# Kernel optimization log

Hardware: AMD Instinct MI355X
Metric: run time of the kernel (lower is better)

The kernel has to match this reference:

```python
import jax, jax.numpy as jnp
import numpy as np

D_MODEL = 128
N_HEADS = 4
HEAD_DIM = D_MODEL // N_HEADS


def setup_inputs() -> dict:
    key = jax.random.key(0)
    ks = jax.random.split(key, 16)
    s = 0.05
    B, N, T = 1, 1024, 1024
    return {
        "node_states": jax.random.normal(ks[0], (B, N, D_MODEL), jnp.float32),
        "task_features": jax.random.normal(ks[1], (T, D_MODEL), jnp.float32),
        "in_proj_w": jax.random.normal(ks[2], (3 * D_MODEL, D_MODEL), jnp.float32) * s,
        "in_proj_b": jnp.zeros((3 * D_MODEL,), jnp.float32),
        "out_w": jax.random.normal(ks[3], (D_MODEL, D_MODEL), jnp.float32) * s,
        "out_b": jnp.zeros((D_MODEL,), jnp.float32),
        "W1": jax.random.normal(ks[4], (256, 256), jnp.float32) * s,
        "b1": jnp.zeros((256,), jnp.float32),
        "W2": jax.random.normal(ks[5], (128, 256), jnp.float32) * s,
        "b2": jnp.zeros((128,), jnp.float32),
        "W3": jax.random.normal(ks[6], (1, 128), jnp.float32) * s,
        "b3": jnp.zeros((1,), jnp.float32),
        "Wc1": jax.random.normal(ks[7], (256, D_MODEL), jnp.float32) * s,
        "bc1": jnp.zeros((256,), jnp.float32),
        "Wc2": jax.random.normal(ks[8], (32, 256), jnp.float32) * s,
        "bc2": jnp.zeros((32,), jnp.float32),
    }


def _mha(x, in_proj_w, in_proj_b, out_w, out_b):
    # x: [B, N, D]; torch nn.MultiheadAttention self-attention, batch_first.
    B, N, D = x.shape
    q = x @ in_proj_w[:D].T + in_proj_b[:D]
    k = x @ in_proj_w[D:2 * D].T + in_proj_b[D:2 * D]
    v = x @ in_proj_w[2 * D:].T + in_proj_b[2 * D:]
    def split(t):  # [B,N,D] -> [B,H,N,dh]
        return t.reshape(B, N, N_HEADS, HEAD_DIM).transpose(0, 2, 1, 3)
    qh, kh, vh = split(q), split(k), split(v)
    scores = jnp.einsum("bhqd,bhkd->bhqk", qh, kh) / jnp.sqrt(jnp.float32(HEAD_DIM))
    attn = jax.nn.softmax(scores, axis=-1)  # [B,H,N,N]
    ctx = jnp.einsum("bhqk,bhkd->bhqd", attn, vh)
    ctx = ctx.transpose(0, 2, 1, 3).reshape(B, N, D)
    out = ctx @ out_w.T + out_b
    attn_avg = attn.mean(axis=1)  # torch averages heads by default -> [B,N,N]
    return out, attn_avg


def reference(node_states, task_features, in_proj_w, in_proj_b, out_w, out_b,
              W1, b1, W2, b2, W3, b3, Wc1, bc1, Wc2, bc2):
    attended, attn_w = _mha(node_states, in_proj_w, in_proj_b, out_w, out_b)
    nodes = attended[0]  # original loop only uses batch 0: [N, D]
    # Linear on concat([task, node]) == split-weight sum; vectorize pairwise.
    t1 = task_features @ W1[:, :D_MODEL].T          # [T, 256]
    n1 = nodes @ W1[:, D_MODEL:].T                  # [N, 256]
    h1 = jax.nn.relu(t1[:, None, :] + n1[None, :, :] + b1)      # [T, N, 256]
    h2 = jax.nn.relu(jnp.einsum("tnc,kc->tnk", h1, W2) + b2)   # [T, N, 128]
    matching_scores = jax.nn.sigmoid(jnp.einsum("tnk,ok->tn", h2, W3) + b3[0])
    global_state = attended.mean(axis=1)            # [B, D]
    coordination_logits = jax.nn.relu(global_state @ Wc1.T + bc1) @ Wc2.T + bc2
    return matching_scores, coordination_logits, attn_w
```

## Files before the change

### kernel.cpp

```cpp
#include <hip/hip_runtime.h>
#include <hip/hip_fp16.h>
#include <stdint.h>


typedef __attribute__((ext_vector_type(4))) float floatx4;
typedef __attribute__((ext_vector_type(8))) _Float16 half8;

#define OFF_QKV  0x000000u
#define OFF_CTX  0x180000u
#define OFF_T1H  0x280000u
#define OFF_N1H  0x300000u
#define OFF_W2F  0x380000u
#define OFF_GS   0x398000u
#define OFF_SC   0x400000u
#define OFF_PG   0xC00000u

__device__ __forceinline__ unsigned pkadd(unsigned a, unsigned b) {
    unsigned r; asm("v_pk_add_f16 %0, %1, %2" : "=v"(r) : "v"(a), "v"(b)); return r;
}
__device__ __forceinline__ unsigned pkmax(unsigned a, unsigned b) {
    unsigned r; asm("v_pk_max_f16 %0, %1, %2" : "=v"(r) : "v"(a), "v"(b)); return r;
}
__device__ __forceinline__ unsigned pk2h(float a, float b) {
    return (unsigned)__half_as_ushort(__float2half(a)) |
           ((unsigned)__half_as_ushort(__float2half(b)) << 16);
}
__device__ __forceinline__ float h2f(unsigned short u) {
    return __half2float(__ushort_as_half(u));
}

template<bool BIAS, bool F16OUT>
__device__ __forceinline__ void gemm_dev(
    const float* __restrict__ A, int lda,
    const float* __restrict__ B, int ldb,
    const float* __restrict__ bias,
    void* __restrict__ Cv, int ldc, int K, float scale,
    int m0, int n0, float (*As)[64], float (*Bs)[64])
{
    const int tid = threadIdx.x;
    const int tx = tid & 15, ty = tid >> 4;
    const int lr = tid >> 2;
    const int lk = (tid & 3) * 4;
    float c[4][4] = {};

    for (int k0 = 0; k0 < K; k0 += 16) {
        float4 a  = *(const float4*)&A[(long)(m0 + lr) * lda + k0 + lk];
        float4 bb = *(const float4*)&B[(long)(n0 + lr) * ldb + k0 + lk];
        __syncthreads();
        As[lk + 0][lr] = a.x;  As[lk + 1][lr] = a.y;  As[lk + 2][lr] = a.z;  As[lk + 3][lr] = a.w;
        Bs[lk + 0][lr] = bb.x; Bs[lk + 1][lr] = bb.y; Bs[lk + 2][lr] = bb.z; Bs[lk + 3][lr] = bb.w;
        __syncthreads();
#pragma unroll
        for (int k = 0; k < 16; k++) {
            float4 av = *(const float4*)&As[k][ty * 4];
            float4 bv = *(const float4*)&Bs[k][tx * 4];
            c[0][0] += av.x * bv.x; c[0][1] += av.x * bv.y; c[0][2] += av.x * bv.z; c[0][3] += av.x * bv.w;
            c[1][0] += av.y * bv.x; c[1][1] += av.y * bv.y; c[1][2] += av.y * bv.z; c[1][3] += av.y * bv.w;
            c[2][0] += av.z * bv.x; c[2][1] += av.z * bv.y; c[2][2] += av.z * bv.z; c[2][3] += av.z * bv.w;
            c[3][0] += av.w * bv.x; c[3][1] += av.w * bv.y; c[3][2] += av.w * bv.z; c[3][3] += av.w * bv.w;
        }
    }

    float bsv[4] = {0.f, 0.f, 0.f, 0.f};
    if (BIAS) {
        float4 t = *(const float4*)&bias[n0 + tx * 4];
        bsv[0] = t.x; bsv[1] = t.y; bsv[2] = t.z; bsv[3] = t.w;
    }
#pragma unroll
    for (int i = 0; i < 4; i++) {
        float v0 = c[i][0] * scale + bsv[0];
        float v1 = c[i][1] * scale + bsv[1];
        float v2 = c[i][2] * scale + bsv[2];
        float v3 = c[i][3] * scale + bsv[3];
        long m = m0 + ty * 4 + i;
        if (F16OUT) {
            unsigned short* Cp = (unsigned short*)Cv;
            ushort4 o;
            o.x = __half_as_ushort(__float2half(v0));
            o.y = __half_as_ushort(__float2half(v1));
            o.z = __half_as_ushort(__float2half(v2));
            o.w = __half_as_ushort(__float2half(v3));
            *(ushort4*)&Cp[m * ldc + n0 + tx * 4] = o;
        } else {
            float* Cp = (float*)Cv;
            *(float4*)&Cp[m * ldc + n0 + tx * 4] = make_float4(v0, v1, v2, v3);
        }
    }
}

__launch_bounds__(256)
__global__ void proj_fused(const float* __restrict__ node, const float* __restrict__ ipw,
                           const float* __restrict__ ipb,
                           const float* __restrict__ task, const float* __restrict__ W1,
                           const float* __restrict__ b1, const float* __restrict__ W2,
                           float* __restrict__ qkv, unsigned short* __restrict__ t1h,
                           unsigned short* __restrict__ w2f, float* __restrict__ gs)
{
    __shared__ float As[16][64], Bs[16][64];
    const int bid = blockIdx.x;
    if (bid < 96) {
        gemm_dev<true, false>(node, 128, ipw, 128, ipb, qkv, 384, 128, 1.0f,
                              (bid & 15) * 64, (bid >> 4) * 64, As, Bs);
    } else if (bid < 160) {
        const int b = bid - 96;
        gemm_dev<true, true>(task, 128, W1, 256, b1, t1h, 256, 128, 1.0f,
                             (b & 15) * 64, (b >> 4) * 64, As, Bs);
    } else if (bid < 176) {
        const int gtid = (bid - 160) * 256 + threadIdx.x;
        const int lane = gtid & 63, frag = gtid >> 6;
        const int cc = frag >> 3, ot = frag & 7;
        const float* src = &W2[(ot * 16 + (lane & 15)) * 256 + cc * 32 + (lane >> 4) * 8];
        uint4 o;
        o.x = pk2h(src[0], src[1]);
        o.y = pk2h(src[2], src[3]);
        o.z = pk2h(src[4], src[5]);
        o.w = pk2h(src[6], src[7]);
        ((uint4*)w2f)[gtid] = o;
    } else {
        if (threadIdx.x < 128) gs[threadIdx.x] = 0.f;
    }
}

__launch_bounds__(256)
__global__ void scores_kernel(const float* __restrict__ qkv, unsigned short* __restrict__ sc16)
{
    __shared__ float As[16][64], Bs[16][64];
    const int h = blockIdx.z;
    gemm_dev<false, true>(qkv + h * 32, 384, qkv + 128 + h * 32, 384, nullptr,
                          sc16 + ((size_t)h << 20), 1024, 32, 0.17677669529663687f,
                          blockIdx.x * 64, blockIdx.y * 64, As, Bs);
}

__launch_bounds__(256)
__global__ void attn_pre(const unsigned short* __restrict__ sc16,
                         unsigned short* __restrict__ Pg, float* __restrict__ attn_out)
{
    __shared__ float Ps[4][1024];
    __shared__ float stm[4], stl[4];
    const int t = threadIdx.x;
    const int q = blockIdx.x;

#pragma unroll
    for (int h = 0; h < 4; h++) {
        ushort4 u = *(const ushort4*)&sc16[((size_t)h << 20) + (size_t)q * 1024 + t * 4];
        float4 f = make_float4(h2f(u.x), h2f(u.y), h2f(u.z), h2f(u.w));
        *(float4*)&Ps[h][t * 4] = f;
    }
    __syncthreads();

    {
        const int h = t >> 6, ln = t & 63;
        float4 v[4];
        float mx = -1e30f;
#pragma unroll
        for (int i = 0; i < 4; i++) {
            v[i] = *(const float4*)&Ps[h][ln * 4 + i * 256];
            mx = fmaxf(mx, fmaxf(fmaxf(v[i].x, v[i].y), fmaxf(v[i].z, v[i].w)));
        }
#pragma unroll
        for (int m = 1; m < 64; m <<= 1) mx = fmaxf(mx, __shfl_xor(mx, m));
        float s = 0.f;
#pragma unroll
        for (int i = 0; i < 4; i++)
            s += __expf(v[i].x - mx) + __expf(v[i].y - mx) +
                 __expf(v[i].z - mx) + __expf(v[i].w - mx);
#pragma unroll
        for (int m = 1; m < 64; m <<= 1) s += __shfl_xor(s, m);
        if (ln == 0) { stm[h] = mx; stl[h] = s; }
    }
    __syncthreads();

    float a0 = 0.f, a1 = 0.f, a2 = 0.f, a3 = 0.f;
#pragma unroll
    for (int h = 0; h < 4; h++) {
        const float m = stm[h], il = 1.0f / stl[h];
        float4 f = *(const float4*)&Ps[h][t * 4];
        float p0 = __expf(f.x - m) * il, p1 = __expf(f.y - m) * il;
        float p2 = __expf(f.z - m) * il, p3 = __expf(f.w - m) * il;
        ushort4 o;
        o.x = __half_as_ushort(__float2half(p0));
        o.y = __half_as_ushort(__float2half(p1));
        o.z = __half_as_ushort(__float2half(p2));
        o.w = __half_as_ushort(__float2half(p3));
        *(ushort4*)&Pg[((size_t)h << 20) + (size_t)q * 1024 + t * 4] = o;
        a0 += p0; a1 += p1; a2 += p2; a3 += p3;
    }
    *(float4*)&attn_out[(size_t)q * 1024 + t * 4] =
        make_float4(0.25f * a0, 0.25f * a1, 0.25f * a2, 0.25f * a3);
}

__launch_bounds__(256)
__global__ void ctx_kernel(const unsigned short* __restrict__ Pg,
                           const float* __restrict__ qkv, float* __restrict__ ctx)
{
    const int h = blockIdx.z;
    const int q0 = blockIdx.x * 64;
    const int kbase = blockIdx.y * 128;
    __shared__ float As[32][64];
    __shared__ float Vs[32][32];
    const int tid = threadIdx.x;
    const int tx = tid & 15, ty = tid >> 4;
    const int sq = tid >> 3;
    const int sk4 = (tid & 7) * 4;
    float acc[4][2] = {};

    for (int k0 = kbase; k0 < kbase + 128; k0 += 32) {
        __syncthreads();
#pragma unroll
        for (int half = 0; half < 2; half++) {
            int q = sq + half * 32;
            ushort4 u = *(const ushort4*)&Pg[((size_t)h << 20) + (size_t)(q0 + q) * 1024 + k0 + sk4];
            As[sk4 + 0][q] = h2f(u.x);
            As[sk4 + 1][q] = h2f(u.y);
            As[sk4 + 2][q] = h2f(u.z);
            As[sk4 + 3][q] = h2f(u.w);
        }
        *(float4*)&Vs[sq][sk4] = *(const float4*)&qkv[(long)(k0 + sq) * 384 + 256 + h * 32 + sk4];
        __syncthreads();
#pragma unroll
        for (int k = 0; k < 32; k++) {
            float4 a = *(const float4*)&As[k][tx * 4];
            float b0 = Vs[k][ty * 2], b1 = Vs[k][ty * 2 + 1];
            acc[0][0] += a.x * b0; acc[0][1] += a.x * b1;
            acc[1][0] += a.y * b0; acc[1][1] += a.y * b1;
            acc[2][0] += a.z * b0; acc[2][1] += a.z * b1;
            acc[3][0] += a.w * b0; acc[3][1] += a.w * b1;
        }
    }
#pragma unroll
    for (int i = 0; i < 4; i++) {
        atomicAdd(&ctx[(long)(q0 + tx * 4 + i) * 128 + h * 32 + ty * 2 + 0], acc[i][0]);
        atomicAdd(&ctx[(long)(q0 + tx * 4 + i) * 128 + h * 32 + ty * 2 + 1], acc[i][1]);
    }
}

__launch_bounds__(256)
__global__ void attn_post(const float* __restrict__ ctx, const float* __restrict__ outw,
                          const float* __restrict__ outb, const float* __restrict__ W1,
                          unsigned short* __restrict__ n1h, float* __restrict__ gs)
{
    __shared__ float ctxs[4][128];
    __shared__ float attr[4][128];
    const int t = threadIdx.x;
    const int q0 = blockIdx.x * 4;

    *(float2*)&ctxs[0][0] + 0;
    {
        float2 v = *(const float2*)&ctx[(size_t)q0 * 128 + t * 2];
        ((float2*)&ctxs[0][0])[t] = v;
    }
    __syncthreads();

    {
        const int j = t & 127, qp = t >> 7;
        float a0 = outb[j], a1 = a0;
        const float* wr = &outw[j * 128];
        for (int d = 0; d < 128; d += 4) {
            float4 w  = *(const float4*)&wr[d];
            float4 c0 = *(const float4*)&ctxs[qp * 2 + 0][d];
            float4 c1 = *(const float4*)&ctxs[qp * 2 + 1][d];
            a0 += w.x * c0.x + w.y * c0.y + w.z * c0.z + w.w * c0.w;
            a1 += w.x * c1.x + w.y * c1.y + w.z * c1.z + w.w * c1.w;
        }
        attr[qp * 2 + 0][j] = a0;
        attr[qp * 2 + 1][j] = a1;
    }
    __syncthreads();
    if (t < 128) atomicAdd(&gs[t], attr[0][t] + attr[1][t] + attr[2][t] + attr[3][t]);

    {
        const int c = t;
        const float* wr = &W1[c * 256 + 128];
        float n[4] = {};
        for (int d = 0; d < 128; d += 4) {
            float4 w = *(const float4*)&wr[d];
#pragma unroll
            for (int q = 0; q < 4; q++) {
                float4 a = *(const float4*)&attr[q][d];
                n[q] += w.x * a.x + w.y * a.y + w.z * a.z + w.w * a.w;
            }
        }
#pragma unroll
        for (int q = 0; q < 4; q++)
            n1h[(size_t)(q0 + q) * 256 + c] = __half_as_ushort(__float2half(n[q]));
    }
}

__launch_bounds__(256, 2)
__global__ void score_kernel(const unsigned short* __restrict__ t1h,
                             const unsigned short* __restrict__ n1h,
                             const unsigned short* __restrict__ w2f,
                             const float* __restrict__ b2, const float* __restrict__ W3,
                             const float* __restrict__ b3, float* __restrict__ out,
                             const float* __restrict__ gs,
                             const float* __restrict__ Wc1, const float* __restrict__ bc1,
                             const float* __restrict__ Wc2, const float* __restrict__ bc2,
                             float* __restrict__ outc)
{
    __shared__ unsigned short w2s[32768];
    __shared__ float b2s[128], w3s[128];
    const int tid = threadIdx.x;

    if (blockIdx.y == 32) {
        if (blockIdx.x != 0) return;
        float* g  = (float*)w2s;
        float* hh = g + 128;
        if (tid < 128) g[tid] = gs[tid] * (1.0f / 1024.0f);
        __syncthreads();
        {
            float a = bc1[tid];
            const float* wr = &Wc1[tid * 128];
            for (int d = 0; d < 128; d += 4) {
                float4 w = *(const float4*)&wr[d];
                a += w.x * g[d] + w.y * g[d + 1] + w.z * g[d + 2] + w.w * g[d + 3];
            }
            hh[tid] = fmaxf(a, 0.f);
        }
        __syncthreads();
        if (tid < 32) {
            float a = bc2[tid];
            const float* wr = &Wc2[tid * 256];
            for (int c = 0; c < 256; c += 4) {
                float4 w = *(const float4*)&wr[c];
                a += w.x * hh[c] + w.y * hh[c + 1] + w.z * hh[c + 2] + w.w * hh[c + 3];
            }
            outc[tid] = a;
        }
        return;
    }

    const int lane = tid & 63;
    const int wv = tid >> 6;
    const int col = lane & 15;
    const int quad = lane >> 4;
    const int nb = blockIdx.x * 64 + wv * 16;
    const int tb = blockIdx.y * 32;

    {
        const uint4* src = (const uint4*)w2f;
        uint4* dst = (uint4*)w2s;
#pragma unroll
        for (int i = 0; i < 16; i++) dst[tid + i * 256] = src[tid + i * 256];
        if (tid < 128) { b2s[tid] = b2[tid]; w3s[tid] = W3[tid]; }
    }

    const int myn = nb + col;
    uint4 n1p[8];
#pragma unroll
    for (int cc = 0; cc < 8; cc++)
        n1p[cc] = *(const uint4*)(n1h + (size_t)myn * 256 + cc * 32 + quad * 8);

    const float b3s = b3[0];
    __syncthreads();

    for (int tg = 0; tg < 8; tg++) {
        floatx4 acc[4][8] = {};

#pragma unroll
        for (int cc = 0; cc < 8; cc++) {
            uint4 tp[4];
#pragma unroll
            for (int tt = 0; tt < 4; tt++)
                tp[tt] = *(const uint4*)(t1h + (size_t)(tb + tg * 4 + tt) * 256 + cc * 32 + quad * 8);

            const unsigned* npu = (const unsigned*)&n1p[cc];
            union { unsigned u[4]; half8 h; } af[4];
#pragma unroll
            for (int tt = 0; tt < 4; tt++) {
                const unsigned* tpu = (const unsigned*)&tp[tt];
#pragma unroll
                for (int p = 0; p < 4; p++)
                    af[tt].u[p] = pkmax(pkadd(tpu[p], npu[p]), 0u);
            }
#pragma unroll
            for (int ot = 0; ot < 8; ot++) {
                union { uint4 u; half8 h; } bf;
                bf.u = *(const uint4*)&w2s[((cc * 8 + ot) * 64 + lane) * 8];
#pragma unroll
                for (int tt = 0; tt < 4; tt++)
                    acc[tt][ot] = __builtin_amdgcn_mfma_f32_16x16x32_f16(bf.h, af[tt].h, acc[tt][ot], 0, 0, 0);
            }
        }

        float part[4] = {0.f, 0.f, 0.f, 0.f};
#pragma unroll
        for (int ot = 0; ot < 8; ot++) {
            float4 bq = *(const float4*)&b2s[ot * 16 + quad * 4];
            float4 wq = *(const float4*)&w3s[ot * 16 + quad * 4];
#pragma unroll
            for (int tt = 0; tt < 4; tt++) {
                floatx4 a = acc[tt][ot];
                part[tt] += fmaxf(a[0] + bq.x, 0.f) * wq.x + fmaxf(a[1] + bq.y, 0.f) * wq.y
                          + fmaxf(a[2] + bq.z, 0.f) * wq.z + fmaxf(a[3] + bq.w, 0.f) * wq.w;
            }
        }
        float outv = 0.f;
#pragma unroll
        for (int tt = 0; tt < 4; tt++) {
            float p = part[tt];
            p += __shfl_xor(p, 16);
            p += __shfl_xor(p, 32);
            if (quad == tt) outv = p;
        }
        out[(size_t)(tb + tg * 4 + quad) * 1024 + nb + col] =
            1.0f / (1.0f + __expf(-(outv + b3s)));
    }
}

extern "C" void kernel_launch(void* const* d_in, const int* in_sizes, int n_in,
                              void* d_out, int out_size, void* d_ws, size_t ws_size,
                              hipStream_t stream)
{
    const float* node = (const float*)d_in[0];
    const float* task = (const float*)d_in[1];
    const float* ipw  = (const float*)d_in[2];
    const float* ipb  = (const float*)d_in[3];
    const float* outw = (const float*)d_in[4];
    const float* outb = (const float*)d_in[5];
    const float* W1   = (const float*)d_in[6];
    const float* b1   = (const float*)d_in[7];
    const float* W2   = (const float*)d_in[8];
    const float* b2   = (const float*)d_in[9];
    const float* W3   = (const float*)d_in[10];
    const float* b3   = (const float*)d_in[11];
    const float* Wc1  = (const float*)d_in[12];
    const float* bc1  = (const float*)d_in[13];
    const float* Wc2  = (const float*)d_in[14];
    const float* bc2  = (const float*)d_in[15];

    char* ws = (char*)d_ws;
    float* qkv = (float*)(ws + OFF_QKV);
    float* ctx = (float*)(ws + OFF_CTX);
    unsigned short* t1h = (unsigned short*)(ws + OFF_T1H);
    unsigned short* n1h = (unsigned short*)(ws + OFF_N1H);
    unsigned short* w2f = (unsigned short*)(ws + OFF_W2F);
    float* gs = (float*)(ws + OFF_GS);
    unsigned short* sc16 = (unsigned short*)(ws + OFF_SC);
    unsigned short* Pg   = (unsigned short*)(ws + OFF_PG);

    float* out_match = (float*)d_out;
    float* out_coord = out_match + 1048576;
    float* out_attn  = out_coord + 32;

    hipMemsetAsync(ctx, 0, 1024 * 128 * 4, stream);
    proj_fused<<<dim3(177, 1, 1), 256, 0, stream>>>(
        node, ipw, ipb, task, W1, b1, W2, qkv, t1h, w2f, gs);
    scores_kernel<<<dim3(16, 16, 4), 256, 0, stream>>>(qkv, sc16);
    attn_pre<<<dim3(1024, 1, 1), 256, 0, stream>>>(sc16, Pg, out_attn);
    ctx_kernel<<<dim3(16, 8, 4), 256, 0, stream>>>(Pg, qkv, ctx);
    attn_post<<<dim3(256, 1, 1), 256, 0, stream>>>(ctx, outw, outb, W1, n1h, gs);
    score_kernel<<<dim3(16, 33, 1), 256, 0, stream>>>(
        t1h, n1h, w2f, b2, W3, b3, out_match,
        gs, Wc1, bc1, Wc2, bc2, out_coord);
}
```

Before: 212.6 us.

## Recompute softmax probabilities in ctx kernel and split score MLP across wave pairs

attn_pre no longer writes the normalized fp16 probability tensor. It stores per-row max and sum, and ctx_kernel recomputes exp(score-m)/l from the fp16 scores, which removes an 8MB write and reread. ctx zeroing moves into attn_pre in place of a separate memset. score_kernel now splits the 128 output channels across pairs of waves, each handling 8 task rows, and combines the partial W3 dot products through shared memory. The grid doubles in x, presumably to raise parallelism or reduce register pressure, at the cost of extra syncs and repeated exp work in ctx_kernel.

```diff
diff --git a/kernel.cpp b/kernel.cpp
--- a/kernel.cpp
+++ b/kernel.cpp
@@ -12,8 +12,9 @@
 #define OFF_N1H  0x300000u
 #define OFF_W2F  0x380000u
 #define OFF_GS   0x398000u
+#define OFF_SM   0x3A0000u
+#define OFF_SL   0x3A8000u
 #define OFF_SC   0x400000u
-#define OFF_PG   0xC00000u
 
 __device__ __forceinline__ unsigned pkadd(unsigned a, unsigned b) {
     unsigned r; asm("v_pk_add_f16 %0, %1, %2" : "=v"(r) : "v"(a), "v"(b)); return r;
@@ -133,7 +134,8 @@
 
 __launch_bounds__(256)
 __global__ void attn_pre(const unsigned short* __restrict__ sc16,
-                         unsigned short* __restrict__ Pg, float* __restrict__ attn_out)
+                         float* __restrict__ sm, float* __restrict__ sl,
+                         float* __restrict__ attn_out, float* __restrict__ ctx)
 {
     __shared__ float Ps[4][1024];
     __shared__ float stm[4], stl[4];
@@ -143,9 +145,9 @@
 #pragma unroll
     for (int h = 0; h < 4; h++) {
         ushort4 u = *(const ushort4*)&sc16[((size_t)h << 20) + (size_t)q * 1024 + t * 4];
-        float4 f = make_float4(h2f(u.x), h2f(u.y), h2f(u.z), h2f(u.w));
-        *(float4*)&Ps[h][t * 4] = f;
-    }
+        *(float4*)&Ps[h][t * 4] = make_float4(h2f(u.x), h2f(u.y), h2f(u.z), h2f(u.w));
+    }
+    if (t < 128) ctx[(size_t)q * 128 + t] = 0.f;
     __syncthreads();
 
     {
@@ -166,7 +168,10 @@
                  __expf(v[i].z - mx) + __expf(v[i].w - mx);
 #pragma unroll
         for (int m = 1; m < 64; m <<= 1) s += __shfl_xor(s, m);
-        if (ln == 0) { stm[h] = mx; stl[h] = s; }
+        if (ln == 0) {
+            stm[h] = mx; stl[h] = s;
+            sm[h * 1024 + q] = mx; sl[h * 1024 + q] = s;
+        }
     }
     __syncthreads();
 
@@ -175,22 +180,18 @@
     for (int h = 0; h < 4; h++) {
         const float m = stm[h], il = 1.0f / stl[h];
         float4 f = *(const float4*)&Ps[h][t * 4];
-        float p0 = __expf(f.x - m) * il, p1 = __expf(f.y - m) * il;
-        float p2 = __expf(f.z - m) * il, p3 = __expf(f.w - m) * il;
-        ushort4 o;
-        o.x = __half_as_ushort(__float2half(p0));
-        o.y = __half_as_ushort(__float2half(p1));
-        o.z = __half_as_ushort(__float2half(p2));
-        o.w = __half_as_ushort(__float2half(p3));
-        *(ushort4*)&Pg[((size_t)h << 20) + (size_t)q * 1024 + t * 4] = o;
-        a0 += p0; a1 += p1; a2 += p2; a3 += p3;
+        a0 += __expf(f.x - m) * il;
+        a1 += __expf(f.y - m) * il;
+        a2 += __expf(f.z - m) * il;
+        a3 += __expf(f.w - m) * il;
     }
     *(float4*)&attn_out[(size_t)q * 1024 + t * 4] =
         make_float4(0.25f * a0, 0.25f * a1, 0.25f * a2, 0.25f * a3);
 }
 
 __launch_bounds__(256)
-__global__ void ctx_kernel(const unsigned short* __restrict__ Pg,
+__global__ void ctx_kernel(const unsigned short* __restrict__ sc16,
+                           const float* __restrict__ sm, const float* __restrict__ sl,
                            const float* __restrict__ qkv, float* __restrict__ ctx)
 {
     const int h = blockIdx.z;
@@ -209,11 +210,13 @@
 #pragma unroll
         for (int half = 0; half < 2; half++) {
             int q = sq + half * 32;
-            ushort4 u = *(const ushort4*)&Pg[((size_t)h << 20) + (size_t)(q0 + q) * 1024 + k0 + sk4];
-            As[sk4 + 0][q] = h2f(u.x);
-            As[sk4 + 1][q] = h2f(u.y);
-            As[sk4 + 2][q] = h2f(u.z);
-            As[sk4 + 3][q] = h2f(u.w);
+            float m = sm[h * 1024 + q0 + q];
+            float il = 1.0f / sl[h * 1024 + q0 + q];
+            ushort4 u = *(const ushort4*)&sc16[((size_t)h << 20) + (size_t)(q0 + q) * 1024 + k0 + sk4];
+            As[sk4 + 0][q] = __expf(h2f(u.x) - m) * il;
+            As[sk4 + 1][q] = __expf(h2f(u.y) - m) * il;
+            As[sk4 + 2][q] = __expf(h2f(u.z) - m) * il;
+            As[sk4 + 3][q] = __expf(h2f(u.w) - m) * il;
         }
         *(float4*)&Vs[sq][sk4] = *(const float4*)&qkv[(long)(k0 + sq) * 384 + 256 + h * 32 + sk4];
         __syncthreads();
@@ -244,7 +247,6 @@
     const int t = threadIdx.x;
     const int q0 = blockIdx.x * 4;
 
-    *(float2*)&ctxs[0][0] + 0;
     {
         float2 v = *(const float2*)&ctx[(size_t)q0 * 128 + t * 2];
         ((float2*)&ctxs[0][0])[t] = v;
@@ -298,6 +300,7 @@
                              float* __restrict__ outc)
 {
     __shared__ unsigned short w2s[32768];
+    __shared__ float pp[4][8][16];
     __shared__ float b2s[128], w3s[128];
     const int tid = threadIdx.x;
 
@@ -331,9 +334,11 @@
 
     const int lane = tid & 63;
     const int wv = tid >> 6;
+    const int pair = wv >> 1;
+    const int half = wv & 1;
     const int col = lane & 15;
     const int quad = lane >> 4;
-    const int nb = blockIdx.x * 64 + wv * 16;
+    const int nb = blockIdx.x * 32 + pair * 16;
     const int tb = blockIdx.y * 32;
 
     {
@@ -353,57 +358,69 @@
     const float b3s = b3[0];
     __syncthreads();
 
-    for (int tg = 0; tg < 8; tg++) {
-        floatx4 acc[4][8] = {};
+    for (int tg = 0; tg < 4; tg++) {
+        floatx4 acc[8][4] = {};
 
 #pragma unroll
         for (int cc = 0; cc < 8; cc++) {
-            uint4 tp[4];
-#pragma unroll
-            for (int tt = 0; tt < 4; tt++)
-                tp[tt] = *(const uint4*)(t1h + (size_t)(tb + tg * 4 + tt) * 256 + cc * 32 + quad * 8);
+            uint4 tp[8];
+#pragma unroll
+            for (int tt = 0; tt < 8; tt++)
+                tp[tt] = *(const uint4*)(t1h + (size_t)(tb + tg * 8 + tt) * 256 + cc * 32 + quad * 8);
 
             const unsigned* npu = (const unsigned*)&n1p[cc];
-            union { unsigned u[4]; half8 h; } af[4];
-#pragma unroll
-            for (int tt = 0; tt < 4; tt++) {
+            union { unsigned u[4]; half8 h; } af[8];
+#pragma unroll
+            for (int tt = 0; tt < 8; tt++) {
                 const unsigned* tpu = (const unsigned*)&tp[tt];
 #pragma unroll
                 for (int p = 0; p < 4; p++)
                     af[tt].u[p] = pkmax(pkadd(tpu[p], npu[p]), 0u);
             }
 #pragma unroll
-            for (int ot = 0; ot < 8; ot++) {
+            for (int oi = 0; oi < 4; oi++) {
                 union { uint4 u; half8 h; } bf;
-                bf.u = *(const uint4*)&w2s[((cc * 8 + ot) * 64 + lane) * 8];
-#pragma unroll
-                for (int tt = 0; tt < 4; tt++)
-                    acc[tt][ot] = __builtin_amdgcn_mfma_f32_16x16x32_f16(bf.h, af[tt].h, acc[tt][ot], 0, 0, 0);
-            }
-        }
-
-        float part[4] = {0.f, 0.f, 0.f, 0.f};
-#pragma unroll
-        for (int ot = 0; ot < 8; ot++) {
-            float4 bq = *(const float4*)&b2s[ot * 16 + quad * 4];
-            float4 wq = *(const float4*)&w3s[ot * 16 + quad * 4];
-#pragma unroll
-            for (int tt = 0; tt < 4; tt++) {
-                floatx4 a = acc[tt][ot];
-                part[tt] += fmaxf(a[0] + bq.x, 0.f) * wq.x + fmaxf(a[1] + bq.y, 0.f) * wq.y
-                          + fmaxf(a[2] + bq.z, 0.f) * wq.z + fmaxf(a[3] + bq.w, 0.f) * wq.w;
-            }
-        }
-        float outv = 0.f;
-#pragma unroll
-        for (int tt = 0; tt < 4; tt++) {
-            float p = part[tt];
-            p += __shfl_xor(p, 16);
-            p += __shfl_xor(p, 32);
-            if (quad == tt) outv = p;
-        }
-        out[(size_t)(tb + tg * 4 + quad) * 1024 + nb + col] =
-            1.0f / (1.0f + __expf(-(outv + b3s)));
+                bf.u = *(const uint4*)&w2s[((cc * 8 + half * 4 + oi) * 64 + lane) * 8];
+#pragma unroll
+                for (int tt = 0; tt < 8; tt++)
+                    acc[tt][oi] = __builtin_amdgcn_mfma_f32_16x16x32_f16(bf.h, af[tt].h, acc[tt][oi], 0, 0, 0);
+            }
+        }
+
+        float p[8] = {};
+#pragma unroll
+        for (int oi = 0; oi < 4; oi++) {
+            float4 bq = *(const float4*)&b2s[(half * 4 + oi) * 16 + quad * 4];
+            float4 wq = *(const float4*)&w3s[(half * 4 + oi) * 16 + quad * 4];
+#pragma unroll
+            for (int tt = 0; tt < 8; tt++) {
+                floatx4 a = acc[tt][oi];
+                p[tt] += fmaxf(a[0] + bq.x, 0.f) * wq.x + fmaxf(a[1] + bq.y, 0.f) * wq.y
+                       + fmaxf(a[2] + bq.z, 0.f) * wq.z + fmaxf(a[3] + bq.w, 0.f) * wq.w;
+            }
+        }
+#pragma unroll
+        for (int tt = 0; tt < 8; tt++) {
+            p[tt] += __shfl_xor(p[tt], 16);
+            p[tt] += __shfl_xor(p[tt], 32);
+        }
+        __syncthreads();
+        {
+            const int tt0 = quad * 2;
+            pp[wv][tt0 + 0][col] = p[tt0 + 0];
+            pp[wv][tt0 + 1][col] = p[tt0 + 1];
+        }
+        __syncthreads();
+        if (half == 0) {
+            const int tt0 = quad * 2;
+#pragma unroll
+            for (int s = 0; s < 2; s++) {
+                const int tt = tt0 + s;
+                float sum = p[tt] + pp[wv + 1][tt][col];
+                out[(size_t)(tb + tg * 8 + tt) * 1024 + nb + col] =
+                    1.0f / (1.0f + __expf(-(sum + b3s)));
+            }
+        }
     }
 }
 
@@ -435,21 +452,21 @@
     unsigned short* n1h = (unsigned short*)(ws + OFF_N1H);
     unsigned short* w2f = (unsigned short*)(ws + OFF_W2F);
     float* gs = (float*)(ws + OFF_GS);
+    float* sm = (float*)(ws + OFF_SM);
+    float* sl = (float*)(ws + OFF_SL);
     unsigned short* sc16 = (unsigned short*)(ws + OFF_SC);
-    unsigned short* Pg   = (unsigned short*)(ws + OFF_PG);
 
     float* out_match = (float*)d_out;
     float* out_coord = out_match + 1048576;
     float* out_attn  = out_coord + 32;
 
-    hipMemsetAsync(ctx, 0, 1024 * 128 * 4, stream);
     proj_fused<<<dim3(177, 1, 1), 256, 0, stream>>>(
         node, ipw, ipb, task, W1, b1, W2, qkv, t1h, w2f, gs);
     scores_kernel<<<dim3(16, 16, 4), 256, 0, stream>>>(qkv, sc16);
-    attn_pre<<<dim3(1024, 1, 1), 256, 0, stream>>>(sc16, Pg, out_attn);
-    ctx_kernel<<<dim3(16, 8, 4), 256, 0, stream>>>(Pg, qkv, ctx);
+    attn_pre<<<dim3(1024, 1, 1), 256, 0, stream>>>(sc16, sm, sl, out_attn, ctx);
+    ctx_kernel<<<dim3(16, 8, 4), 256, 0, stream>>>(sc16, sm, sl, qkv, ctx);
     attn_post<<<dim3(256, 1, 1), 256, 0, stream>>>(ctx, outw, outb, W1, n1h, gs);
-    score_kernel<<<dim3(16, 33, 1), 256, 0, stream>>>(
+    score_kernel<<<dim3(32, 33, 1), 256, 0, stream>>>(
         t1h, n1h, w2f, b2, W3, b3, out_match,
         gs, Wc1, bc1, Wc2, bc2, out_coord);
 }
```

Result: slower. 237.3 us (+11.6%).

## Recompute softmax probabilities in ctx kernel and replace atomics with split-K partials

Applied to the files above, without the earlier changes.

attn_pre no longer writes the fp16 probability matrix (4×1024×1024). It stores only the per-row max and sum, and ctx_kernel recomputes exp(s-m)/l from the fp16 scores as it loads them. The ctx accumulation now writes per-k-split partial buffers instead of doing atomicAdd into a zeroed buffer, which removes the memset. attn_post sums the 8 partials. This saves a large intermediate write and read, plus the memset and atomics, at the cost of extra exp work in ctx_kernel and an 8-way partial read in attn_post.

```diff
diff --git a/kernel.cpp b/kernel.cpp
--- a/kernel.cpp
+++ b/kernel.cpp
@@ -7,13 +7,14 @@
 typedef __attribute__((ext_vector_type(8))) _Float16 half8;
 
 #define OFF_QKV  0x000000u
-#define OFF_CTX  0x180000u
 #define OFF_T1H  0x280000u
 #define OFF_N1H  0x300000u
 #define OFF_W2F  0x380000u
 #define OFF_GS   0x398000u
+#define OFF_SM   0x3A0000u
+#define OFF_SL   0x3A8000u
 #define OFF_SC   0x400000u
-#define OFF_PG   0xC00000u
+#define OFF_CTP  0xC00000u
 
 __device__ __forceinline__ unsigned pkadd(unsigned a, unsigned b) {
     unsigned r; asm("v_pk_add_f16 %0, %1, %2" : "=v"(r) : "v"(a), "v"(b)); return r;
@@ -133,7 +134,8 @@
 
 __launch_bounds__(256)
 __global__ void attn_pre(const unsigned short* __restrict__ sc16,
-                         unsigned short* __restrict__ Pg, float* __restrict__ attn_out)
+                         float* __restrict__ sm, float* __restrict__ sl,
+                         float* __restrict__ attn_out)
 {
     __shared__ float Ps[4][1024];
     __shared__ float stm[4], stl[4];
@@ -143,8 +145,7 @@
 #pragma unroll
     for (int h = 0; h < 4; h++) {
         ushort4 u = *(const ushort4*)&sc16[((size_t)h << 20) + (size_t)q * 1024 + t * 4];
-        float4 f = make_float4(h2f(u.x), h2f(u.y), h2f(u.z), h2f(u.w));
-        *(float4*)&Ps[h][t * 4] = f;
+        *(float4*)&Ps[h][t * 4] = make_float4(h2f(u.x), h2f(u.y), h2f(u.z), h2f(u.w));
     }
     __syncthreads();
 
@@ -166,7 +167,10 @@
                  __expf(v[i].z - mx) + __expf(v[i].w - mx);
 #pragma unroll
         for (int m = 1; m < 64; m <<= 1) s += __shfl_xor(s, m);
-        if (ln == 0) { stm[h] = mx; stl[h] = s; }
+        if (ln == 0) {
+            stm[h] = mx; stl[h] = s;
+            sm[h * 1024 + q] = mx; sl[h * 1024 + q] = s;
+        }
     }
     __syncthreads();
 
@@ -175,27 +179,24 @@
     for (int h = 0; h < 4; h++) {
         const float m = stm[h], il = 1.0f / stl[h];
         float4 f = *(const float4*)&Ps[h][t * 4];
-        float p0 = __expf(f.x - m) * il, p1 = __expf(f.y - m) * il;
-        float p2 = __expf(f.z - m) * il, p3 = __expf(f.w - m) * il;
-        ushort4 o;
-        o.x = __half_as_ushort(__float2half(p0));
-        o.y = __half_as_ushort(__float2half(p1));
-        o.z = __half_as_ushort(__float2half(p2));
-        o.w = __half_as_ushort(__float2half(p3));
-        *(ushort4*)&Pg[((size_t)h << 20) + (size_t)q * 1024 + t * 4] = o;
-        a0 += p0; a1 += p1; a2 += p2; a3 += p3;
+        a0 += __expf(f.x - m) * il;
+        a1 += __expf(f.y - m) * il;
+        a2 += __expf(f.z - m) * il;
+        a3 += __expf(f.w - m) * il;
     }
     *(float4*)&attn_out[(size_t)q * 1024 + t * 4] =
         make_float4(0.25f * a0, 0.25f * a1, 0.25f * a2, 0.25f * a3);
 }
 
 __launch_bounds__(256)
-__global__ void ctx_kernel(const unsigned short* __restrict__ Pg,
-                           const float* __restrict__ qkv, float* __restrict__ ctx)
+__global__ void ctx_kernel(const unsigned short* __restrict__ sc16,
+                           const float* __restrict__ sm, const float* __restrict__ sl,
+                           const float* __restrict__ qkv, float* __restrict__ ctxp)
 {
     const int h = blockIdx.z;
     const int q0 = blockIdx.x * 64;
-    const int kbase = blockIdx.y * 128;
+    const int ks = blockIdx.y;
+    const int kbase = ks * 128;
     __shared__ float As[32][64];
     __shared__ float Vs[32][32];
     const int tid = threadIdx.x;
@@ -209,11 +210,13 @@
 #pragma unroll
         for (int half = 0; half < 2; half++) {
             int q = sq + half * 32;
-            ushort4 u = *(const ushort4*)&Pg[((size_t)h << 20) + (size_t)(q0 + q) * 1024 + k0 + sk4];
-            As[sk4 + 0][q] = h2f(u.x);
-            As[sk4 + 1][q] = h2f(u.y);
-            As[sk4 + 2][q] = h2f(u.z);
-            As[sk4 + 3][q] = h2f(u.w);
+            float m = sm[h * 1024 + q0 + q];
+            float il = 1.0f / sl[h * 1024 + q0 + q];
+            ushort4 u = *(const ushort4*)&sc16[((size_t)h << 20) + (size_t)(q0 + q) * 1024 + k0 + sk4];
+            As[sk4 + 0][q] = __expf(h2f(u.x) - m) * il;
+            As[sk4 + 1][q] = __expf(h2f(u.y) - m) * il;
+            As[sk4 + 2][q] = __expf(h2f(u.z) - m) * il;
+            As[sk4 + 3][q] = __expf(h2f(u.w) - m) * il;
         }
         *(float4*)&Vs[sq][sk4] = *(const float4*)&qkv[(long)(k0 + sq) * 384 + 256 + h * 32 + sk4];
         __syncthreads();
@@ -229,13 +232,13 @@
     }
 #pragma unroll
     for (int i = 0; i < 4; i++) {
-        atomicAdd(&ctx[(long)(q0 + tx * 4 + i) * 128 + h * 32 + ty * 2 + 0], acc[i][0]);
-        atomicAdd(&ctx[(long)(q0 + tx * 4 + i) * 128 + h * 32 + ty * 2 + 1], acc[i][1]);
+        *(float2*)&ctxp[((size_t)ks * 1024 + (q0 + tx * 4 + i)) * 128 + h * 32 + ty * 2] =
+            make_float2(acc[i][0], acc[i][1]);
     }
 }
 
 __launch_bounds__(256)
-__global__ void attn_post(const float* __restrict__ ctx, const float* __restrict__ outw,
+__global__ void attn_post(const float* __restrict__ ctxp, const float* __restrict__ outw,
                           const float* __restrict__ outb, const float* __restrict__ W1,
                           unsigned short* __restrict__ n1h, float* __restrict__ gs)
 {
@@ -244,10 +247,15 @@
     const int t = threadIdx.x;
     const int q0 = blockIdx.x * 4;
 
-    *(float2*)&ctxs[0][0] + 0;
-    {
-        float2 v = *(const float2*)&ctx[(size_t)q0 * 128 + t * 2];
-        ((float2*)&ctxs[0][0])[t] = v;
+#pragma unroll
+    for (int s = 0; s < 2; s++) {
+        const int idx = s * 256 + t;
+        const int q = idx >> 7, d = idx & 127;
+        float v = 0.f;
+#pragma unroll
+        for (int ks = 0; ks < 8; ks++)
+            v += ctxp[((size_t)ks * 1024 + (q0 + q)) * 128 + d];
+        ctxs[q][d] = v;
     }
     __syncthreads();
 
@@ -430,25 +438,25 @@
 
     char* ws = (char*)d_ws;
     float* qkv = (float*)(ws + OFF_QKV);
-    float* ctx = (float*)(ws + OFF_CTX);
     unsigned short* t1h = (unsigned short*)(ws + OFF_T1H);
     unsigned short* n1h = (unsigned short*)(ws + OFF_N1H);
     unsigned short* w2f = (unsigned short*)(ws + OFF_W2F);
     float* gs = (float*)(ws + OFF_GS);
+    float* sm = (float*)(ws + OFF_SM);
+    float* sl = (float*)(ws + OFF_SL);
     unsigned short* sc16 = (unsigned short*)(ws + OFF_SC);
-    unsigned short* Pg   = (unsigned short*)(ws + OFF_PG);
+    float* ctxp = (float*)(ws + OFF_CTP);
 
     float* out_match = (float*)d_out;
     float* out_coord = out_match + 1048576;
     float* out_attn  = out_coord + 32;
 
-    hipMemsetAsync(ctx, 0, 1024 * 128 * 4, stream);
     proj_fused<<<dim3(177, 1, 1), 256, 0, stream>>>(
         node, ipw, ipb, task, W1, b1, W2, qkv, t1h, w2f, gs);
     scores_kernel<<<dim3(16, 16, 4), 256, 0, stream>>>(qkv, sc16);
-    attn_pre<<<dim3(1024, 1, 1), 256, 0, stream>>>(sc16, Pg, out_attn);
-    ctx_kernel<<<dim3(16, 8, 4), 256, 0, stream>>>(Pg, qkv, ctx);
-    attn_post<<<dim3(256, 1, 1), 256, 0, stream>>>(ctx, outw, outb, W1, n1h, gs);
+    attn_pre<<<dim3(1024, 1, 1), 256, 0, stream>>>(sc16, sm, sl, out_attn);
+    ctx_kernel<<<dim3(16, 8, 4), 256, 0, stream>>>(sc16, sm, sl, qkv, ctxp);
+    attn_post<<<dim3(256, 1, 1), 256, 0, stream>>>(ctxp, outw, outb, W1, n1h, gs);
     score_kernel<<<dim3(16, 33, 1), 256, 0, stream>>>(
         t1h, n1h, w2f, b2, W3, b3, out_match,
         gs, Wc1, bc1, Wc2, bc2, out_coord);
```

Result: faster. 195.9 us (-7.9%).
